# Kernel tuning notes

Measured on AMD Instinct MI355X. Metric: run time of the kernel, lower is better.

The kernel has to match this reference:

```python
import jax, jax.numpy as jnp
import numpy as np

PAGE = 16  # page_size hard-coded in the torch module's forward


def setup_inputs() -> dict:
    rng = np.random.default_rng(0)
    B = 4096
    pre = rng.integers(0, 4096, size=B).astype(np.int32)
    ext = rng.integers(1, 8192, size=B).astype(np.int32)
    seq = (pre + ext).astype(np.int32)
    # last token slot of the existing prefix (identity layout); -1 when pre==0
    # (kernel never reads it in that case since num_part1 == 0).
    last_loc = (pre - 1).astype(np.int32)
    free_page = rng.permutation(2_097_152).astype(np.int32)
    return {
        "pre_lens": jnp.asarray(pre),
        "seq_lens": jnp.asarray(seq),
        "last_loc": jnp.asarray(last_loc),
        "free_page": jnp.asarray(free_page),
    }


def reference(pre_lens, seq_lens, last_loc, free_page):
    ext = seq_lens - pre_lens                      # [B] extend length per seq
    cum = jnp.cumsum(ext)                          # inclusive prefix sum
    starts = cum - ext                             # exclusive prefix sum = output_start_loc
    total = int(cum[-1])                           # total extend tokens (static given setup)

    pages_before = (pre_lens + PAGE - 1) // PAGE   # ceil(pre/page)
    pages_after = (seq_lens + PAGE - 1) // PAGE    # ceil(seq/page)
    new_pages = pages_after - pages_before
    new_start = jnp.cumsum(new_pages) - new_pages  # new_page_start_loc per seq

    # Per-token flat computation (replaces the per-program scatter):
    t = jnp.arange(total, dtype=jnp.int32)
    seg = jnp.searchsorted(cum, t, side="right").astype(jnp.int32)  # owning sequence
    o = t - starts[seg]                            # offset within this seq's extend
    p = pre_lens[seg] + o                          # absolute position in sequence

    # part1: tokens filling the existing partially-used page -> contiguous after last_loc
    boundary = pages_before[seg] * PAGE            # ceil(pre/page)*page
    in_part1 = p < boundary
    val1 = last_loc[seg] + 1 + o

    # part2/part3: tokens on newly allocated pages pulled from free_page
    k = p // PAGE - pages_before[seg]              # which new page (>=0 when not part1)
    idx = jnp.clip(new_start[seg] + k, 0, free_page.shape[0] - 1)
    val2 = free_page[idx] * PAGE + p % PAGE

    return jnp.where(in_part1, val1, val2).astype(jnp.int32)
```

## Files before the change

kernel.cpp:

```cpp
#include <hip/hip_runtime.h>

#define PAGE_SHIFT 4
#define PAGE_MASK 15

__global__ __launch_bounds__(1024) void scan_kernel(const int* __restrict__ pre_lens,
                                                    const int* __restrict__ seq_lens,
                                                    int B,
                                                    int* __restrict__ starts,
                                                    int* __restrict__ new_start) {
    __shared__ int s_ext[1024];
    __shared__ int s_np[1024];
    const int t = threadIdx.x;

    int e[4], np[4];
    int sum_e = 0, sum_np = 0;
#pragma unroll
    for (int j = 0; j < 4; ++j) {
        int i = t * 4 + j;
        int pe = (i < B) ? pre_lens[i] : 0;
        int se = (i < B) ? seq_lens[i] : 0;
        int ex = se - pe;
        int pb = (pe + PAGE_MASK) >> PAGE_SHIFT;
        int pa = (se + PAGE_MASK) >> PAGE_SHIFT;
        e[j] = ex;
        np[j] = pa - pb;
        sum_e += ex;
        sum_np += np[j];
    }
    s_ext[t] = sum_e;
    s_np[t] = sum_np;
    __syncthreads();

    for (int off = 1; off < 1024; off <<= 1) {
        int ve = 0, vn = 0;
        if (t >= off) { ve = s_ext[t - off]; vn = s_np[t - off]; }
        __syncthreads();
        s_ext[t] += ve;
        s_np[t] += vn;
        __syncthreads();
    }

    int base_e = (t > 0) ? s_ext[t - 1] : 0;
    int base_n = (t > 0) ? s_np[t - 1] : 0;
#pragma unroll
    for (int j = 0; j < 4; ++j) {
        int i = t * 4 + j;
        if (i < B) {
            starts[i] = base_e;
            new_start[i] = base_n;
        }
        base_e += e[j];
        base_n += np[j];
    }
}

__global__ __launch_bounds__(256) void assign_kernel(const int* __restrict__ pre_lens,
                                                     const int* __restrict__ seq_lens,
                                                     const int* __restrict__ last_loc,
                                                     const int* __restrict__ free_page,
                                                     const int* __restrict__ starts,
                                                     const int* __restrict__ new_start,
                                                     int* __restrict__ out,
                                                     int n_free) {
    const int b = blockIdx.x;
    const int pre = pre_lens[b];
    const int seqv = seq_lens[b];
    const int ext = seqv - pre;
    const int start = starts[b];
    const int ll1 = last_loc[b] + 1;
    const int pb = (pre + PAGE_MASK) >> PAGE_SHIFT;
    const int boundary = pb << PAGE_SHIFT;
    const int ns = new_start[b];

    for (int o = threadIdx.x; o < ext; o += blockDim.x) {
        int p = pre + o;
        int v;
        if (p < boundary) {
            v = ll1 + o;
        } else {
            int k = (p >> PAGE_SHIFT) - pb;
            int idx = ns + k;
            idx = min(max(idx, 0), n_free - 1);
            v = free_page[idx] * (1 << PAGE_SHIFT) + (p & PAGE_MASK);
        }
        out[start + o] = v;
    }
}

extern "C" void kernel_launch(void* const* d_in, const int* in_sizes, int n_in,
                              void* d_out, int out_size, void* d_ws, size_t ws_size,
                              hipStream_t stream) {
    const int* pre_lens  = (const int*)d_in[0];
    const int* seq_lens  = (const int*)d_in[1];
    const int* last_loc  = (const int*)d_in[2];
    const int* free_page = (const int*)d_in[3];
    const int B = in_sizes[0];
    const int n_free = in_sizes[3];

    int* starts    = (int*)d_ws;
    int* new_start = ((int*)d_ws) + B;

    scan_kernel<<<1, 1024, 0, stream>>>(pre_lens, seq_lens, B, starts, new_start);
    assign_kernel<<<B, 256, 0, stream>>>(pre_lens, seq_lens, last_loc, free_page,
                                         starts, new_start, (int*)d_out, n_free);
}
```

Measured before the change: 106.8 us.

## Split per-sequence token assignment across a 2D grid with vectorized stores

The assign kernel now launches a B x 8 grid. Each block handles a 1024-token tile of one sequence, and threads compute four consecutive slots and write them as an int4. A small prologue handles the unaligned head so the vector stores line up on 16-byte boundaries. The single-block scan replaces its shared-memory Hillis-Steele loop with wavefront shuffle scans plus a cross-wave step, and loads and stores through int4. The goal is more parallelism for long sequences and fewer, wider memory transactions, at the cost of many idle blocks for short sequences and repeated per-block setup loads.

Result: faster. 102.3 us (-4.2%).

```diff
diff --git a/kernel.cpp b/kernel.cpp
--- a/kernel.cpp
+++ b/kernel.cpp
@@ -2,56 +2,98 @@
 
 #define PAGE_SHIFT 4
 #define PAGE_MASK 15
+#define TOK_PER_BLOCK 1024
+#define MAX_EXT_TILES 8
 
 __global__ __launch_bounds__(1024) void scan_kernel(const int* __restrict__ pre_lens,
                                                     const int* __restrict__ seq_lens,
                                                     int B,
                                                     int* __restrict__ starts,
                                                     int* __restrict__ new_start) {
-    __shared__ int s_ext[1024];
-    __shared__ int s_np[1024];
+    __shared__ int w_e[16];
+    __shared__ int w_n[16];
     const int t = threadIdx.x;
+    const int lane = t & 63;
+    const int wv = t >> 6;
+    const int i0 = t * 4;
+
+    int pe[4], se[4];
+    if (i0 + 3 < B) {
+        int4 pv = *reinterpret_cast<const int4*>(pre_lens + i0);
+        int4 sv = *reinterpret_cast<const int4*>(seq_lens + i0);
+        pe[0] = pv.x; pe[1] = pv.y; pe[2] = pv.z; pe[3] = pv.w;
+        se[0] = sv.x; se[1] = sv.y; se[2] = sv.z; se[3] = sv.w;
+    } else {
+#pragma unroll
+        for (int j = 0; j < 4; ++j) {
+            pe[j] = (i0 + j < B) ? pre_lens[i0 + j] : 0;
+            se[j] = (i0 + j < B) ? seq_lens[i0 + j] : 0;
+        }
+    }
 
     int e[4], np[4];
-    int sum_e = 0, sum_np = 0;
+    int tot_e = 0, tot_n = 0;
 #pragma unroll
     for (int j = 0; j < 4; ++j) {
-        int i = t * 4 + j;
-        int pe = (i < B) ? pre_lens[i] : 0;
-        int se = (i < B) ? seq_lens[i] : 0;
-        int ex = se - pe;
-        int pb = (pe + PAGE_MASK) >> PAGE_SHIFT;
-        int pa = (se + PAGE_MASK) >> PAGE_SHIFT;
-        e[j] = ex;
+        e[j] = se[j] - pe[j];
+        int pb = (pe[j] + PAGE_MASK) >> PAGE_SHIFT;
+        int pa = (se[j] + PAGE_MASK) >> PAGE_SHIFT;
         np[j] = pa - pb;
-        sum_e += ex;
-        sum_np += np[j];
+        tot_e += e[j];
+        tot_n += np[j];
     }
-    s_ext[t] = sum_e;
-    s_np[t] = sum_np;
+
+    int sc_e = tot_e, sc_n = tot_n;
+#pragma unroll
+    for (int d = 1; d < 64; d <<= 1) {
+        int ve = __shfl_up(sc_e, d, 64);
+        int vn = __shfl_up(sc_n, d, 64);
+        if (lane >= d) { sc_e += ve; sc_n += vn; }
+    }
+    if (lane == 63) { w_e[wv] = sc_e; w_n[wv] = sc_n; }
     __syncthreads();
 
-    for (int off = 1; off < 1024; off <<= 1) {
-        int ve = 0, vn = 0;
-        if (t >= off) { ve = s_ext[t - off]; vn = s_np[t - off]; }
-        __syncthreads();
-        s_ext[t] += ve;
-        s_np[t] += vn;
-        __syncthreads();
+    if (wv == 0) {
+        int ve = (lane < 16) ? w_e[lane] : 0;
+        int vn = (lane < 16) ? w_n[lane] : 0;
+#pragma unroll
+        for (int d = 1; d < 16; d <<= 1) {
+            int ae = __shfl_up(ve, d, 64);
+            int an = __shfl_up(vn, d, 64);
+            if (lane >= d) { ve += ae; vn += an; }
+        }
+        if (lane < 16) { w_e[lane] = ve; w_n[lane] = vn; }
     }
+    __syncthreads();
 
-    int base_e = (t > 0) ? s_ext[t - 1] : 0;
-    int base_n = (t > 0) ? s_np[t - 1] : 0;
+    int base_e = (wv > 0 ? w_e[wv - 1] : 0) + (sc_e - tot_e);
+    int base_n = (wv > 0 ? w_n[wv - 1] : 0) + (sc_n - tot_n);
+
+    if (i0 + 3 < B) {
+        int4 oe, on;
+        oe.x = base_e;            on.x = base_n;
+        oe.y = oe.x + e[0];       on.y = on.x + np[0];
+        oe.z = oe.y + e[1];       on.z = on.y + np[1];
+        oe.w = oe.z + e[2];       on.w = on.z + np[2];
+        *reinterpret_cast<int4*>(starts + i0) = oe;
+        *reinterpret_cast<int4*>(new_start + i0) = on;
+    } else {
 #pragma unroll
-    for (int j = 0; j < 4; ++j) {
-        int i = t * 4 + j;
-        if (i < B) {
-            starts[i] = base_e;
-            new_start[i] = base_n;
+        for (int j = 0; j < 4; ++j) {
+            if (i0 + j < B) { starts[i0 + j] = base_e; new_start[i0 + j] = base_n; }
+            base_e += e[j];
+            base_n += np[j];
         }
-        base_e += e[j];
-        base_n += np[j];
     }
+}
+
+__device__ __forceinline__ int slot_value(int o, int pre, int boundary, int pb, int ll1,
+                                          int ns, const int* __restrict__ fp, int n_free) {
+    int p = pre + o;
+    if (p < boundary) return ll1 + o;
+    int idx = ns + (p >> PAGE_SHIFT) - pb;
+    idx = min(max(idx, 0), n_free - 1);
+    return fp[idx] * (1 << PAGE_SHIFT) + (p & PAGE_MASK);
 }
 
 __global__ __launch_bounds__(256) void assign_kernel(const int* __restrict__ pre_lens,
@@ -64,26 +106,41 @@
                                                      int n_free) {
     const int b = blockIdx.x;
     const int pre = pre_lens[b];
-    const int seqv = seq_lens[b];
-    const int ext = seqv - pre;
+    const int ext = seq_lens[b] - pre;
     const int start = starts[b];
-    const int ll1 = last_loc[b] + 1;
-    const int pb = (pre + PAGE_MASK) >> PAGE_SHIFT;
-    const int boundary = pb << PAGE_SHIFT;
-    const int ns = new_start[b];
+    const int al = (-start) & 3;
+    const int ty = blockIdx.y;
 
-    for (int o = threadIdx.x; o < ext; o += blockDim.x) {
-        int p = pre + o;
-        int v;
-        if (p < boundary) {
-            v = ll1 + o;
+    for (int obase = al + ty * TOK_PER_BLOCK; ; obase += gridDim.y * TOK_PER_BLOCK) {
+        bool any = (obase < ext) || (ty == 0 && obase == al);
+        if (!any) return;
+
+        const int ll1 = last_loc[b] + 1;
+        const int pb = (pre + PAGE_MASK) >> PAGE_SHIFT;
+        const int boundary = pb << PAGE_SHIFT;
+        const int ns = new_start[b];
+
+        if (ty == 0 && obase == al) {
+            int o = (int)threadIdx.x;
+            if (o < al && o < ext) {
+                out[start + o] = slot_value(o, pre, boundary, pb, ll1, ns, free_page, n_free);
+            }
+        }
+
+        int o = obase + (int)threadIdx.x * 4;
+        if (o + 3 < ext) {
+            int4 v;
+            v.x = slot_value(o,     pre, boundary, pb, ll1, ns, free_page, n_free);
+            v.y = slot_value(o + 1, pre, boundary, pb, ll1, ns, free_page, n_free);
+            v.z = slot_value(o + 2, pre, boundary, pb, ll1, ns, free_page, n_free);
+            v.w = slot_value(o + 3, pre, boundary, pb, ll1, ns, free_page, n_free);
+            *reinterpret_cast<int4*>(out + start + o) = v;
         } else {
-            int k = (p >> PAGE_SHIFT) - pb;
-            int idx = ns + k;
-            idx = min(max(idx, 0), n_free - 1);
-            v = free_page[idx] * (1 << PAGE_SHIFT) + (p & PAGE_MASK);
+            for (int oo = o; oo < ext; ++oo) {
+                out[start + oo] = slot_value(oo, pre, boundary, pb, ll1, ns, free_page, n_free);
+            }
         }
-        out[start + o] = v;
+        if (obase + gridDim.y * TOK_PER_BLOCK >= ext) return;
     }
 }
 
@@ -101,6 +158,7 @@
     int* new_start = ((int*)d_ws) + B;
 
     scan_kernel<<<1, 1024, 0, stream>>>(pre_lens, seq_lens, B, starts, new_start);
-    assign_kernel<<<B, 256, 0, stream>>>(pre_lens, seq_lens, last_loc, free_page,
-                                         starts, new_start, (int*)d_out, n_free);
+    dim3 grid(B, MAX_EXT_TILES);
+    assign_kernel<<<grid, 256, 0, stream>>>(pre_lens, seq_lens, last_loc, free_page,
+                                            starts, new_start, (int*)d_out, n_free);
 }
```
